# Performance work log

Hardware: AMD Instinct MI355X
Metric: run time of the kernel (lower is better)

## Reference

```python
import jax, jax.numpy as jnp
import numpy as np

LAMBDA_COLOR = 0.01
BLUR = 0.01          # geomloss blur
P = 2                # geomloss p
EPS_FINAL = BLUR ** P  # 1e-4
# Note: with scaling=1.2 (>1), geomloss's epsilon_schedule arange is empty, so
# eps_list = [diameter**p, blur**p] -> exactly two annealing stages.


def cost_matrix(x, y, lambda_color):
    # x: [B,N,6], y: [B,M,6]
    cx, col_x = x[..., :3], x[..., 3:]
    cy, col_y = y[..., :3], y[..., 3:]
    max_norm = jnp.max(jnp.linalg.norm(jnp.concatenate([cx, cy], axis=1), axis=-1))
    s = 1.0 / (max_norm + 1e-6)
    cxn, cyn = cx * s, cy * s
    coord = jnp.sum((cxn[:, :, None, :] - cyn[:, None, :, :]) ** 2, axis=-1)  # [B,N,M]
    col_x = jnp.clip(col_x, 0.0, 1.0)
    col_y = jnp.clip(col_y, 0.0, 1.0)
    col = jnp.sum((col_x[:, :, None, :] - col_y[:, None, :, :]) ** 2, axis=-1)
    return jnp.maximum(coord + lambda_color * col, 0.0)


def softmin(eps, C, h):
    # h: [B,M] = log_weights + potential/eps ; C: [B,N,M]
    return -eps * jax.nn.logsumexp(h[:, None, :] - C / eps, axis=2)  # [B,N]


def sinkhorn_distance(x, y, lambda_color):
    B, N, _ = x.shape
    M = y.shape[1]
    a_log = jnp.full((B, N), -np.log(N), dtype=x.dtype)
    b_log = jnp.full((B, M), -np.log(M), dtype=x.dtype)

    C_xy = cost_matrix(x, y, lambda_color)          # [B,N,M]
    C_yx = jnp.swapaxes(C_xy, 1, 2)                 # cost is symmetric in x<->y

    # diameter over raw 6-d features (geomloss max_diameter)
    pts = jnp.concatenate([x.reshape(-1, x.shape[-1]), y.reshape(-1, y.shape[-1])], axis=0)
    diameter = jnp.linalg.norm(pts.max(0) - pts.min(0))
    eps_list = (diameter ** P, jnp.asarray(EPS_FINAL, x.dtype))

    # Sinkhorn loop runs without gradient through the potentials (geomloss semantics)
    Cs_xy = jax.lax.stop_gradient(C_xy)
    Cs_yx = jax.lax.stop_gradient(C_yx)

    eps = eps_list[0]
    f = softmin(eps, Cs_xy, b_log)   # potential on x
    g = softmin(eps, Cs_yx, a_log)   # potential on y
    for eps in eps_list:
        ft = softmin(eps, Cs_xy, b_log + g / eps)
        gt = softmin(eps, Cs_yx, a_log + f / eps)
        f, g = 0.5 * (f + ft), 0.5 * (g + gt)

    # final extrapolation with gradient-carrying cost, detached dual potentials
    eps = eps_list[-1]
    f_new = softmin(eps, C_xy, b_log + jax.lax.stop_gradient(g) / eps)
    g_new = softmin(eps, C_yx, a_log + jax.lax.stop_gradient(f) / eps)

    # <a,f> + <b,g> with uniform weights
    ot = f_new.mean(axis=1) + g_new.mean(axis=1)   # [B]
    return ot.mean() * 10.0


def setup_inputs() -> dict:
    key = jax.random.key(0)
    kx, ky = jax.random.split(key)
    x = jax.random.normal(kx, (4, 4096, 6), dtype=jnp.float32)
    y = jax.random.normal(ky, (4, 4096, 6), dtype=jnp.float32)
    return {"x": x, "y": y}


def reference(x, y):
    return sinkhorn_distance(x, y, LAMBDA_COLOR)
```

## Files before the change

### kernel.cpp

```cpp
#include <hip/hip_runtime.h>

#define ROWS 16384
#define PTS_TOTAL 32768
#define NSM_BLK 512

#define LOG2E 1.4426950408889634f
#define LN2   0.6931471805599453f
#define NEG_LOG2M (-12.0f)
#define EPS1LNM 8.317766166719343e-4f

typedef _Float16 h2 __attribute__((ext_vector_type(2)));
typedef _Float16 v8h __attribute__((ext_vector_type(8)));
typedef float f32x4 __attribute__((ext_vector_type(4)));

__device__ inline float fexp2(float x) { return __builtin_amdgcn_exp2f(x); }
__device__ inline float flog2(float x) { return __builtin_amdgcn_logf(x); }

__device__ inline unsigned fenc(float f) {
  unsigned u = __float_as_uint(f);
  return (u & 0x80000000u) ? ~u : (u | 0x80000000u);
}
__device__ inline float fdec(unsigned u) {
  return (u & 0x80000000u) ? __uint_as_float(u & 0x7fffffffu)
                           : __uint_as_float(~u);
}
__device__ inline unsigned pkh2(float a, float b) {
  h2 hv; hv.x = (_Float16)a; hv.y = (_Float16)b;
  return __builtin_bit_cast(unsigned, hv);
}
__device__ inline v8h bcv8(uint4 u) { return __builtin_bit_cast(v8h, u); }

__device__ inline float mkv(const float* __restrict__ p, float s, float* v) {
  v[0] = p[0] * s; v[1] = p[1] * s; v[2] = p[2] * s;
  v[3] = 0.1f * fminf(fmaxf(p[3], 0.0f), 1.0f);
  v[4] = 0.1f * fminf(fmaxf(p[4], 0.0f), 1.0f);
  v[5] = 0.1f * fminf(fmaxf(p[5], 0.0f), 1.0f);
  return v[0]*v[0] + v[1]*v[1] + v[2]*v[2] + v[3]*v[3] + v[4]*v[4] + v[5]*v[5];
}

__device__ inline float taylor_f(const float* __restrict__ M, const float* v,
                                 float q, float eps0) {
  float sc2 = 2.0f * LOG2E / eps0;
  float p[6];
#pragma unroll
  for (int d = 0; d < 6; ++d) p[d] = v[d] * sc2;
  float t1 = 0.0f;
#pragma unroll
  for (int d = 0; d < 6; ++d) t1 += p[d] * M[1 + d];
  float t2 = 0.0f;
  int kk = 7;
#pragma unroll
  for (int d = 0; d < 6; ++d) {
#pragma unroll
    for (int e = d; e < 6; ++e) {
      float coef = (d == e) ? 1.0f : 2.0f;
      t2 += coef * p[d] * p[e] * M[kk];
      kk++;
    }
  }
  float S = M[0] + LN2 * t1 + (0.5f * LN2 * LN2) * t2;
  return q - eps0 * LN2 * flog2(S);
}

__device__ inline void mom28(float* acc, float wgt, const float* v) {
  acc[0] = wgt;
  int kk = 1;
#pragma unroll
  for (int d = 0; d < 6; ++d) acc[kk++] = wgt * v[d];
#pragma unroll
  for (int d = 0; d < 6; ++d) {
    float wv = wgt * v[d];
#pragma unroll
    for (int e = d; e < 6; ++e) acc[kk++] = wv * v[e];
  }
}

__device__ inline void red28g(float* acc, float* __restrict__ dst,
                              float (*shf)[28], int t, int wave, int lane) {
#pragma unroll
  for (int off = 32; off > 0; off >>= 1) {
#pragma unroll
    for (int k = 0; k < 28; ++k) acc[k] += __shfl_xor(acc[k], off);
  }
  if (lane == 0) {
#pragma unroll
    for (int k = 0; k < 28; ++k) shf[wave][k] = acc[k];
  }
  __syncthreads();
  if (t < 28) dst[t] = (shf[0][t] + shf[1][t]) + (shf[2][t] + shf[3][t]);
}

__device__ inline void se_from_rmax(const unsigned* __restrict__ RMAXu,
                                    unsigned (*shu)[13], float& s, float& eps0,
                                    int t, int wave, int lane) {
  int set = t & 127;
  unsigned e[13];
#pragma unroll
  for (int k = 0; k < 13; ++k) e[k] = RMAXu[set * 16 + k];
#pragma unroll
  for (int off = 32; off > 0; off >>= 1) {
#pragma unroll
    for (int k = 0; k < 13; ++k) {
      unsigned o = (unsigned)__shfl_xor((int)e[k], off);
      e[k] = e[k] > o ? e[k] : o;
    }
  }
  if (lane == 0) {
#pragma unroll
    for (int k = 0; k < 13; ++k) shu[wave][k] = e[k];
  }
  __syncthreads();
  unsigned mm[13];
#pragma unroll
  for (int k = 0; k < 13; ++k) {
    unsigned v0 = shu[0][k] > shu[1][k] ? shu[0][k] : shu[1][k];
    unsigned v1 = shu[2][k] > shu[3][k] ? shu[2][k] : shu[3][k];
    mm[k] = v0 > v1 ? v0 : v1;
  }
  s = 1.0f / (sqrtf(fdec(mm[0])) + 1e-6f);
  eps0 = 0.0f;
#pragma unroll
  for (int k = 0; k < 6; ++k) {
    float dd = fdec(mm[1 + k]) + fdec(mm[7 + k]);
    eps0 += dd * dd;
  }
}

__global__ __launch_bounds__(256) void k1_max(
    const float* __restrict__ x, const float* __restrict__ y,
    float* __restrict__ w) {
  unsigned* BARC = (unsigned*)w;
  unsigned* RMAX = (unsigned*)w + 64;
  const int t = threadIdx.x, wave = t >> 6, lane = t & 63, bx = blockIdx.x;
  if (bx == 0 && t == 0) BARC[0] = 0u;
  const int g0 = bx * 256;
  bool isx = g0 < ROWS;
  __shared__ float4 st[384];
  const float4* src =
      (const float4*)((isx ? x : y) + (size_t)(g0 & (ROWS - 1)) * 6);
  st[t] = src[t];
  if (t < 128) st[256 + t] = src[256 + t];
  __syncthreads();
  const float* sp = (const float*)st + t * 6;
  float d[6];
#pragma unroll
  for (int k = 0; k < 6; ++k) d[k] = sp[k];
  unsigned e[13];
  e[0] = fenc(d[0] * d[0] + d[1] * d[1] + d[2] * d[2]);
#pragma unroll
  for (int k = 0; k < 6; ++k) {
    e[1 + k] = fenc(d[k]);
    e[7 + k] = fenc(-d[k]);
  }
#pragma unroll
  for (int off = 32; off > 0; off >>= 1) {
#pragma unroll
    for (int k = 0; k < 13; ++k) {
      unsigned o = (unsigned)__shfl_xor((int)e[k], off);
      e[k] = e[k] > o ? e[k] : o;
    }
  }
  __shared__ unsigned shu[4][13];
  if (lane == 0) {
#pragma unroll
    for (int k = 0; k < 13; ++k) shu[wave][k] = e[k];
  }
  __syncthreads();
  if (t < 13) {
    unsigned v = shu[0][t];
#pragma unroll
    for (int wv = 1; wv < 4; ++wv) v = v > shu[wv][t] ? v : shu[wv][t];
    RMAX[bx * 16 + t] = v;
  }
}

__global__ __launch_bounds__(256) void k2_pack(
    const float* __restrict__ x, const float* __restrict__ y,
    float* __restrict__ w) {
  const int t = threadIdx.x, wave = t >> 6, lane = t & 63, bx = blockIdx.x;
  const unsigned* RMAX = (const unsigned*)w + 64;
  float* MOMP1 = w + 2560;
  float* base = w + 16384;
  uint4* AREC = (uint4*)base;
  float* Qarr = base + 3 * 4 * PTS_TOTAL;

  __shared__ unsigned shu[4][13];
  __shared__ float shf[4][28];
  float s, eps0;
  se_from_rmax(RMAX, shu, s, eps0, t, wave, lane);

  const int g = bx * 256 + t;
  const int side = g >> 14;
  const float* p = (side ? y : x) + (size_t)(g & (ROWS - 1)) * 6;
  float v[6]; float q = mkv(p, s, v);
  Qarr[g] = q;
  unsigned w01 = pkh2(v[0], v[1]), w23 = pkh2(v[2], v[3]), w45 = pkh2(v[4], v[5]);
  AREC[g] = (uint4){w01, w23, w45, pkh2(1.0f, 0.0f)};

  float wgt = fexp2(NEG_LOG2M - q * (LOG2E / eps0));
  float acc[28];
  mom28(acc, wgt, v);
  red28g(acc, MOMP1 + (size_t)bx * 32, shf, t, wave, lane);
}

__global__ __launch_bounds__(256) void k3_rows1(
    const float* __restrict__ x, const float* __restrict__ y,
    float* __restrict__ w) {
  const int t = threadIdx.x, wave = t >> 6, lane = t & 63, bx = blockIdx.x;
  const unsigned* RMAX = (const unsigned*)w + 64;
  const float* MOMP1 = w + 2560;
  float* MOMP2 = w + 2560 + 4096;
  float* base = w + 16384;
  float* FG1 = base + 3 * 4 * PTS_TOTAL + PTS_TOTAL + PTS_TOTAL;

  __shared__ unsigned shu[4][13];
  __shared__ float shf[4][28];
  __shared__ float M1opp[28];
  float s, eps0;
  se_from_rmax(RMAX, shu, s, eps0, t, wave, lane);

  const int g = bx * 256 + t;
  const int side = g >> 14;
  const int batch = (g >> 12) & 3;
  if (t < 28) {
    const float* mp = MOMP1 + ((size_t)((side ^ 1) * 64 + batch * 16)) * 32 + t;
    float m = 0.0f;
#pragma unroll
    for (int j = 0; j < 16; ++j) m += mp[j * 32];
    M1opp[t] = m;
  }
  __syncthreads();

  const float* p = (side ? y : x) + (size_t)(g & (ROWS - 1)) * 6;
  float v[6]; float q = mkv(p, s, v);
  float f1 = taylor_f(M1opp, v, q, eps0);
  FG1[g] = f1;
  float w2 = fexp2(NEG_LOG2M + (f1 - q) * (LOG2E / eps0));
  float acc[28];
  mom28(acc, w2, v);
  red28g(acc, MOMP2 + (size_t)bx * 32, shf, t, wave, lane);
}

__global__ __launch_bounds__(256) void k4_rows2(
    const float* __restrict__ x, const float* __restrict__ y,
    float* __restrict__ w) {
  const int t = threadIdx.x, wave = t >> 6, lane = t & 63, bx = blockIdx.x;
  const unsigned* RMAX = (const unsigned*)w + 64;
  const float* MOMP2 = w + 2560 + 4096;
  float* base = w + 16384;
  uint4* BRECA = (uint4*)base + PTS_TOTAL;
  float* Qarr = base + 3 * 4 * PTS_TOTAL;
  float* FG2 = Qarr + PTS_TOTAL;
  const float* FG1 = FG2 + PTS_TOTAL;

  __shared__ unsigned shu[4][13];
  __shared__ float M2opp[28];
  float s, eps0;
  se_from_rmax(RMAX, shu, s, eps0, t, wave, lane);

  const int g = bx * 256 + t;
  const int side = g >> 14;
  const int batch = (g >> 12) & 3;
  if (t < 28) {
    const float* mp = MOMP2 + ((size_t)((side ^ 1) * 64 + batch * 16)) * 32 + t;
    float m = 0.0f;
#pragma unroll
    for (int j = 0; j < 16; ++j) m += mp[j * 32];
    M2opp[t] = m;
  }
  __syncthreads();

  const float* p = (side ? y : x) + (size_t)(g & (ROWS - 1)) * 6;
  float v[6]; float q = mkv(p, s, v);
  float f1 = FG1[g];
  float f_t = taylor_f(M2opp, v, q, eps0);
  float f2 = 0.5f * (f1 + f_t);
  FG2[g] = f2;
  float hs2 = 0.5f * (f2 - q - EPS1LNM);
  unsigned w01 = pkh2(v[0], v[1]), w23 = pkh2(v[2], v[3]), w45 = pkh2(v[4], v[5]);
  BRECA[g] = (uint4){w01, w23, w45, pkh2(hs2, 0.0f)};
}

__device__ inline float softmax_max64L(const uint4* __restrict__ AREC,
                                       const uint4* __restrict__ BIN,
                                       uint4* __restrict__ Blds,
                                       float (*lm)[32]) {
  int t = threadIdx.x;
  int w = t >> 6, lane = t & 63;
  int l16 = lane & 15;
  bool ldq = lane < 16;
  int grow0 = blockIdx.x * 64;
  int side = grow0 >> 14;
  int batch = (grow0 & (ROWS - 1)) >> 12;
  int panel0 = (side ^ 1) * ROWS + batch * 4096;

  const uint4* gsrc = BIN + panel0 + w * 512 + lane;
  uint4* ldst = Blds + w * 512 + lane;
  uint4 s0 = gsrc[0],   s1 = gsrc[64],  s2 = gsrc[128], s3 = gsrc[192];
  uint4 s4 = gsrc[256], s5 = gsrc[320], s6 = gsrc[384], s7 = gsrc[448];

  uint4 z4 = (uint4){0u, 0u, 0u, 0u};
  uint4 a1u = z4, a2u = z4;
  int arow = grow0 + (w >> 2) * 32;
  if (ldq) {
    a1u = AREC[arow + l16];
    a2u = AREC[arow + 16 + l16];
  }
  v8h a1 = bcv8(a1u), a2 = bcv8(a2u);

  ldst[0] = s0;   ldst[64] = s1;  ldst[128] = s2; ldst[192] = s3;
  ldst[256] = s4; ldst[320] = s5; ldst[384] = s6; ldst[448] = s7;
  __syncthreads();

  f32x4 m2a = {-3.0e38f, -3.0e38f, -3.0e38f, -3.0e38f};
  f32x4 m2b = m2a;
  const f32x4 cz = {0.0f, 0.0f, 0.0f, 0.0f};
  const int colq = (w & 3) * 1024;

#pragma unroll 8
  for (int tt = 0; tt < 64; ++tt) {
    uint4 bu = z4;
    if (ldq) bu = Blds[colq + tt * 16 + l16];
    v8h b = bcv8(bu);
    f32x4 d1 = __builtin_amdgcn_mfma_f32_16x16x32_f16(a1, b, cz, 0, 0, 0);
    f32x4 d2 = __builtin_amdgcn_mfma_f32_16x16x32_f16(a2, b, cz, 0, 0, 0);
    m2a = __builtin_elementwise_max(m2a, d1);
    m2b = __builtin_elementwise_max(m2b, d2);
  }

#pragma unroll
  for (int off = 1; off <= 8; off <<= 1) {
#pragma unroll
    for (int r = 0; r < 4; ++r) {
      m2a[r] = fmaxf(m2a[r], __shfl_xor(m2a[r], off));
      m2b[r] = fmaxf(m2b[r], __shfl_xor(m2b[r], off));
    }
  }
  if (l16 == 0) {
    int qd = lane >> 4;
#pragma unroll
    for (int r = 0; r < 4; ++r) {
      lm[w][qd * 4 + r] = m2a[r];
      lm[w][16 + qd * 4 + r] = m2b[r];
    }
  }
  __syncthreads();
  float m = 0.0f;
  if (t < 64) {
    int half4 = (t >> 5) * 4, r32 = t & 31;
    m = fmaxf(fmaxf(lm[half4][r32], lm[half4 + 1][r32]),
              fmaxf(lm[half4 + 2][r32], lm[half4 + 3][r32]));
  }
  return m;
}

__global__ __launch_bounds__(512) void kb_sm1(
    const uint4* __restrict__ AREC, const uint4* __restrict__ BIN,
    uint4* __restrict__ BOUT, const float* __restrict__ Qarr,
    const float* __restrict__ FG2) {
  __shared__ uint4 Blds[4096];
  __shared__ float lm[8][32];
  int t = threadIdx.x;
  int grow0 = blockIdx.x * 64;
  float qv = 0.0f, fprev = 0.0f;
  uint4 ar = (uint4){0u, 0u, 0u, 0u};
  if (t < 64) {
    int gg = grow0 + t;
    qv = Qarr[gg];
    fprev = FG2[gg];
    ar = AREC[gg];
  }
  float m = softmax_max64L(AREC, BIN, Blds, lm);
  if (t < 64) {
    float f_t = qv - 2.0f * m;
    float fo = 0.5f * (fprev + f_t);
    float hs = 0.5f * (fo - qv - EPS1LNM);
    BOUT[grow0 + t] = (uint4){ar.x, ar.y, ar.z, pkh2(hs, 0.0f)};
  }
}

__global__ __launch_bounds__(512) void kc_sm2(
    const uint4* __restrict__ AREC, const uint4* __restrict__ BIN,
    const float* __restrict__ Qarr, float* __restrict__ PART,
    unsigned* __restrict__ BARC, float* __restrict__ out) {
  __shared__ uint4 Blds[4096];
  __shared__ float lm[8][32];
  __shared__ float fsh[64];
  __shared__ float fred[8];
  __shared__ int lastf;
  int t = threadIdx.x;
  int wave = t >> 6, lane = t & 63;
  int grow0 = blockIdx.x * 64;
  float qv = 0.0f;
  if (t < 64) qv = Qarr[grow0 + t];
  float m = softmax_max64L(AREC, BIN, Blds, lm);
  if (t < 64) fsh[t] = qv - 2.0f * m;
  __syncthreads();
  if (t == 0) {
    float ssum = 0.0f;
#pragma unroll
    for (int k = 0; k < 64; ++k) ssum += fsh[k];
    __hip_atomic_store(&PART[blockIdx.x], ssum, __ATOMIC_RELAXED,
                       __HIP_MEMORY_SCOPE_AGENT);
    unsigned old = __hip_atomic_fetch_add(BARC, 1u, __ATOMIC_ACQ_REL,
                                          __HIP_MEMORY_SCOPE_AGENT);
    lastf = (old == (unsigned)(NSM_BLK - 1)) ? 1 : 0;
  }
  __syncthreads();
  if (lastf) {
    float a = __hip_atomic_load(&PART[t], __ATOMIC_RELAXED,
                                __HIP_MEMORY_SCOPE_AGENT);
#pragma unroll
    for (int off = 32; off > 0; off >>= 1) a += __shfl_xor(a, off);
    if (lane == 0) fred[wave] = a;
    __syncthreads();
    if (t == 0) {
      float s8 = 0.0f;
#pragma unroll
      for (int k = 0; k < 8; ++k) s8 += fred[k];
      out[0] = s8 * (10.0f / (float)ROWS);
    }
  }
}

extern "C" void kernel_launch(void* const* d_in, const int* in_sizes, int n_in,
                              void* d_out, int out_size, void* d_ws,
                              size_t ws_size, hipStream_t stream) {
  const float* x = (const float*)d_in[0];
  const float* y = (const float*)d_in[1];
  float* out = (float*)d_out;
  float* w = (float*)d_ws;

  unsigned* BARC = (unsigned*)w;
  float* base = w + 16384;
  uint4* AREC  = (uint4*)base;
  uint4* BRECA = AREC + PTS_TOTAL;
  uint4* BRECB = BRECA + PTS_TOTAL;
  float* Qarr  = base + 3 * 4 * PTS_TOTAL;
  float* FG2   = Qarr + PTS_TOTAL;
  float* FG1   = FG2 + PTS_TOTAL;
  float* PART  = FG1 + PTS_TOTAL;

  (void)ws_size;
  k1_max<<<128, 256, 0, stream>>>(x, y, w);
  k2_pack<<<128, 256, 0, stream>>>(x, y, w);
  k3_rows1<<<128, 256, 0, stream>>>(x, y, w);
  k4_rows2<<<128, 256, 0, stream>>>(x, y, w);
  kb_sm1<<<NSM_BLK, 512, 0, stream>>>(AREC, BRECA, BRECB, Qarr, FG2);
  kc_sm2<<<NSM_BLK, 512, 0, stream>>>(AREC, BRECB, Qarr, PART, BARC, out);
}
```

Baseline: 99.65 us.

## Fuse four preprocessing kernels into one with grid-wide atomic barriers

```diff
diff --git a/kernel.cpp b/kernel.cpp
--- a/kernel.cpp
+++ b/kernel.cpp
@@ -3,6 +3,7 @@
 #define ROWS 16384
 #define PTS_TOTAL 32768
 #define NSM_BLK 512
+#define NEPS_BLK 128
 
 #define LOG2E 1.4426950408889634f
 #define LN2   0.6931471805599453f
@@ -30,11 +31,11 @@
 }
 __device__ inline v8h bcv8(uint4 u) { return __builtin_bit_cast(v8h, u); }
 
-__device__ inline float mkv(const float* __restrict__ p, float s, float* v) {
-  v[0] = p[0] * s; v[1] = p[1] * s; v[2] = p[2] * s;
-  v[3] = 0.1f * fminf(fmaxf(p[3], 0.0f), 1.0f);
-  v[4] = 0.1f * fminf(fmaxf(p[4], 0.0f), 1.0f);
-  v[5] = 0.1f * fminf(fmaxf(p[5], 0.0f), 1.0f);
+__device__ inline float mkv_d(const float* d, float s, float* v) {
+  v[0] = d[0] * s; v[1] = d[1] * s; v[2] = d[2] * s;
+  v[3] = 0.1f * fminf(fmaxf(d[3], 0.0f), 1.0f);
+  v[4] = 0.1f * fminf(fmaxf(d[4], 0.0f), 1.0f);
+  v[5] = 0.1f * fminf(fmaxf(d[5], 0.0f), 1.0f);
   return v[0]*v[0] + v[1]*v[1] + v[2]*v[2] + v[3]*v[3] + v[4]*v[4] + v[5]*v[5];
 }
 
@@ -75,67 +76,50 @@
   }
 }
 
-__device__ inline void red28g(float* acc, float* __restrict__ dst,
-                              float (*shf)[28], int t, int wave, int lane) {
-#pragma unroll
-  for (int off = 32; off > 0; off >>= 1) {
-#pragma unroll
-    for (int k = 0; k < 28; ++k) acc[k] += __shfl_xor(acc[k], off);
-  }
-  if (lane == 0) {
-#pragma unroll
-    for (int k = 0; k < 28; ++k) shf[wave][k] = acc[k];
-  }
-  __syncthreads();
-  if (t < 28) dst[t] = (shf[0][t] + shf[1][t]) + (shf[2][t] + shf[3][t]);
-}
-
-__device__ inline void se_from_rmax(const unsigned* __restrict__ RMAXu,
-                                    unsigned (*shu)[13], float& s, float& eps0,
-                                    int t, int wave, int lane) {
-  int set = t & 127;
-  unsigned e[13];
-#pragma unroll
-  for (int k = 0; k < 13; ++k) e[k] = RMAXu[set * 16 + k];
-#pragma unroll
-  for (int off = 32; off > 0; off >>= 1) {
-#pragma unroll
-    for (int k = 0; k < 13; ++k) {
-      unsigned o = (unsigned)__shfl_xor((int)e[k], off);
-      e[k] = e[k] > o ? e[k] : o;
-    }
-  }
-  if (lane == 0) {
-#pragma unroll
-    for (int k = 0; k < 13; ++k) shu[wave][k] = e[k];
-  }
-  __syncthreads();
-  unsigned mm[13];
-#pragma unroll
-  for (int k = 0; k < 13; ++k) {
-    unsigned v0 = shu[0][k] > shu[1][k] ? shu[0][k] : shu[1][k];
-    unsigned v1 = shu[2][k] > shu[3][k] ? shu[2][k] : shu[3][k];
-    mm[k] = v0 > v1 ? v0 : v1;
-  }
-  s = 1.0f / (sqrtf(fdec(mm[0])) + 1e-6f);
-  eps0 = 0.0f;
-#pragma unroll
-  for (int k = 0; k < 6; ++k) {
-    float dd = fdec(mm[1 + k]) + fdec(mm[7 + k]);
-    eps0 += dd * dd;
-  }
-}
-
-__global__ __launch_bounds__(256) void k1_max(
+__device__ inline void lite_bar(unsigned* c, unsigned n) {
+  __syncthreads();
+  if (threadIdx.x == 0) {
+    __hip_atomic_fetch_add(c, 1u, __ATOMIC_ACQ_REL, __HIP_MEMORY_SCOPE_AGENT);
+    while (__hip_atomic_load(c, __ATOMIC_ACQUIRE, __HIP_MEMORY_SCOPE_AGENT) < n)
+      __builtin_amdgcn_s_sleep(4);
+  }
+  __syncthreads();
+}
+
+__global__ __launch_bounds__(256) void k0_init(float* __restrict__ w) {
+  int t = threadIdx.x;
+  unsigned* u = (unsigned*)w;
+  if (t < 4) u[t] = 0u;
+  if (t < 128) u[64 + t] = 0u;
+  w[2560 + t] = 0.0f;
+  w[2816 + t] = 0.0f;
+}
+
+__global__ __launch_bounds__(256) void k_eps0(
     const float* __restrict__ x, const float* __restrict__ y,
     float* __restrict__ w) {
-  unsigned* BARC = (unsigned*)w;
-  unsigned* RMAX = (unsigned*)w + 64;
   const int t = threadIdx.x, wave = t >> 6, lane = t & 63, bx = blockIdx.x;
-  if (bx == 0 && t == 0) BARC[0] = 0u;
+  unsigned* CNT = (unsigned*)w;
+  unsigned* ENC = (unsigned*)w + 64;
+  float* MOM1 = w + 2560;
+  float* MOM2 = w + 2816;
+  float* base = w + 16384;
+  uint4* AREC  = (uint4*)base;
+  uint4* BRECA = (uint4*)base + PTS_TOTAL;
+  float* Qarr  = base + 3 * 4 * PTS_TOTAL;
+  float* FG2   = Qarr + PTS_TOTAL;
+
+  const int g = bx * 256 + t;
   const int g0 = bx * 256;
+  const int side = g0 >> 14;
+  const int batch = (g0 >> 12) & 3;
+
+  __shared__ float4 st[384];
+  __shared__ unsigned shu[4][13];
+  __shared__ float shf[4][28];
+  __shared__ float Msh[28];
+
   bool isx = g0 < ROWS;
-  __shared__ float4 st[384];
   const float4* src =
       (const float4*)((isx ? x : y) + (size_t)(g0 & (ROWS - 1)) * 6);
   st[t] = src[t];
@@ -145,139 +129,112 @@
   float d[6];
 #pragma unroll
   for (int k = 0; k < 6; ++k) d[k] = sp[k];
-  unsigned e[13];
-  e[0] = fenc(d[0] * d[0] + d[1] * d[1] + d[2] * d[2]);
-#pragma unroll
-  for (int k = 0; k < 6; ++k) {
-    e[1 + k] = fenc(d[k]);
-    e[7 + k] = fenc(-d[k]);
-  }
-#pragma unroll
-  for (int off = 32; off > 0; off >>= 1) {
-#pragma unroll
-    for (int k = 0; k < 13; ++k) {
-      unsigned o = (unsigned)__shfl_xor((int)e[k], off);
-      e[k] = e[k] > o ? e[k] : o;
-    }
-  }
-  __shared__ unsigned shu[4][13];
-  if (lane == 0) {
-#pragma unroll
-    for (int k = 0; k < 13; ++k) shu[wave][k] = e[k];
-  }
-  __syncthreads();
-  if (t < 13) {
-    unsigned v = shu[0][t];
-#pragma unroll
-    for (int wv = 1; wv < 4; ++wv) v = v > shu[wv][t] ? v : shu[wv][t];
-    RMAX[bx * 16 + t] = v;
-  }
-}
-
-__global__ __launch_bounds__(256) void k2_pack(
-    const float* __restrict__ x, const float* __restrict__ y,
-    float* __restrict__ w) {
-  const int t = threadIdx.x, wave = t >> 6, lane = t & 63, bx = blockIdx.x;
-  const unsigned* RMAX = (const unsigned*)w + 64;
-  float* MOMP1 = w + 2560;
-  float* base = w + 16384;
-  uint4* AREC = (uint4*)base;
-  float* Qarr = base + 3 * 4 * PTS_TOTAL;
-
-  __shared__ unsigned shu[4][13];
-  __shared__ float shf[4][28];
+  {
+    unsigned e[13];
+    e[0] = fenc(d[0] * d[0] + d[1] * d[1] + d[2] * d[2]);
+#pragma unroll
+    for (int k = 0; k < 6; ++k) {
+      e[1 + k] = fenc(d[k]);
+      e[7 + k] = fenc(-d[k]);
+    }
+#pragma unroll
+    for (int off = 32; off > 0; off >>= 1) {
+#pragma unroll
+      for (int k = 0; k < 13; ++k) {
+        unsigned o = (unsigned)__shfl_xor((int)e[k], off);
+        e[k] = e[k] > o ? e[k] : o;
+      }
+    }
+    if (lane == 0) {
+#pragma unroll
+      for (int k = 0; k < 13; ++k) shu[wave][k] = e[k];
+    }
+    __syncthreads();
+    if (t < 13) {
+      unsigned v = shu[0][t];
+#pragma unroll
+      for (int wv = 1; wv < 4; ++wv) v = v > shu[wv][t] ? v : shu[wv][t];
+      atomicMax(&ENC[t * 8], v);
+    }
+  }
+  lite_bar(CNT + 0, NEPS_BLK);
+  if (t < 13)
+    shu[0][t] = __hip_atomic_load(&ENC[t * 8], __ATOMIC_RELAXED,
+                                  __HIP_MEMORY_SCOPE_AGENT);
+  __syncthreads();
   float s, eps0;
-  se_from_rmax(RMAX, shu, s, eps0, t, wave, lane);
-
-  const int g = bx * 256 + t;
-  const int side = g >> 14;
-  const float* p = (side ? y : x) + (size_t)(g & (ROWS - 1)) * 6;
-  float v[6]; float q = mkv(p, s, v);
+  {
+    s = 1.0f / (sqrtf(fdec(shu[0][0])) + 1e-6f);
+    eps0 = 0.0f;
+#pragma unroll
+    for (int k = 0; k < 6; ++k) {
+      float dd = fdec(shu[0][1 + k]) + fdec(shu[0][7 + k]);
+      eps0 += dd * dd;
+    }
+  }
+
+  float v[6];
+  float q = mkv_d(d, s, v);
+  {
+    float wgt = fexp2(NEG_LOG2M - q * (LOG2E / eps0));
+    float acc[28];
+    mom28(acc, wgt, v);
+#pragma unroll
+    for (int off = 32; off > 0; off >>= 1) {
+#pragma unroll
+      for (int k = 0; k < 28; ++k) acc[k] += __shfl_xor(acc[k], off);
+    }
+    if (lane == 0) {
+#pragma unroll
+      for (int k = 0; k < 28; ++k) shf[wave][k] = acc[k];
+    }
+    __syncthreads();
+    if (t < 28) {
+      float vv = (shf[0][t] + shf[1][t]) + (shf[2][t] + shf[3][t]);
+      __hip_atomic_fetch_add(&MOM1[(side * 4 + batch) * 32 + t], vv,
+                             __ATOMIC_RELAXED, __HIP_MEMORY_SCOPE_AGENT);
+    }
+  }
+  lite_bar(CNT + 1, NEPS_BLK);
+  if (t < 28)
+    Msh[t] = __hip_atomic_load(&MOM1[((side ^ 1) * 4 + batch) * 32 + t],
+                               __ATOMIC_RELAXED, __HIP_MEMORY_SCOPE_AGENT);
+  __syncthreads();
+  float f1 = taylor_f(Msh, v, q, eps0);
+
+  {
+    float w2 = fexp2(NEG_LOG2M + (f1 - q) * (LOG2E / eps0));
+    float acc[28];
+    mom28(acc, w2, v);
+#pragma unroll
+    for (int off = 32; off > 0; off >>= 1) {
+#pragma unroll
+      for (int k = 0; k < 28; ++k) acc[k] += __shfl_xor(acc[k], off);
+    }
+    if (lane == 0) {
+#pragma unroll
+      for (int k = 0; k < 28; ++k) shf[wave][k] = acc[k];
+    }
+    __syncthreads();
+    if (t < 28) {
+      float vv = (shf[0][t] + shf[1][t]) + (shf[2][t] + shf[3][t]);
+      __hip_atomic_fetch_add(&MOM2[(side * 4 + batch) * 32 + t], vv,
+                             __ATOMIC_RELAXED, __HIP_MEMORY_SCOPE_AGENT);
+    }
+  }
+  lite_bar(CNT + 2, NEPS_BLK);
+  if (t < 28)
+    Msh[t] = __hip_atomic_load(&MOM2[((side ^ 1) * 4 + batch) * 32 + t],
+                               __ATOMIC_RELAXED, __HIP_MEMORY_SCOPE_AGENT);
+  __syncthreads();
+
+  float f_t = taylor_f(Msh, v, q, eps0);
+  float f2 = 0.5f * (f1 + f_t);
   Qarr[g] = q;
+  FG2[g] = f2;
   unsigned w01 = pkh2(v[0], v[1]), w23 = pkh2(v[2], v[3]), w45 = pkh2(v[4], v[5]);
   AREC[g] = (uint4){w01, w23, w45, pkh2(1.0f, 0.0f)};
-
-  float wgt = fexp2(NEG_LOG2M - q * (LOG2E / eps0));
-  float acc[28];
-  mom28(acc, wgt, v);
-  red28g(acc, MOMP1 + (size_t)bx * 32, shf, t, wave, lane);
-}
-
-__global__ __launch_bounds__(256) void k3_rows1(
-    const float* __restrict__ x, const float* __restrict__ y,
-    float* __restrict__ w) {
-  const int t = threadIdx.x, wave = t >> 6, lane = t & 63, bx = blockIdx.x;
-  const unsigned* RMAX = (const unsigned*)w + 64;
-  const float* MOMP1 = w + 2560;
-  float* MOMP2 = w + 2560 + 4096;
-  float* base = w + 16384;
-  float* FG1 = base + 3 * 4 * PTS_TOTAL + PTS_TOTAL + PTS_TOTAL;
-
-  __shared__ unsigned shu[4][13];
-  __shared__ float shf[4][28];
-  __shared__ float M1opp[28];
-  float s, eps0;
-  se_from_rmax(RMAX, shu, s, eps0, t, wave, lane);
-
-  const int g = bx * 256 + t;
-  const int side = g >> 14;
-  const int batch = (g >> 12) & 3;
-  if (t < 28) {
-    const float* mp = MOMP1 + ((size_t)((side ^ 1) * 64 + batch * 16)) * 32 + t;
-    float m = 0.0f;
-#pragma unroll
-    for (int j = 0; j < 16; ++j) m += mp[j * 32];
-    M1opp[t] = m;
-  }
-  __syncthreads();
-
-  const float* p = (side ? y : x) + (size_t)(g & (ROWS - 1)) * 6;
-  float v[6]; float q = mkv(p, s, v);
-  float f1 = taylor_f(M1opp, v, q, eps0);
-  FG1[g] = f1;
-  float w2 = fexp2(NEG_LOG2M + (f1 - q) * (LOG2E / eps0));
-  float acc[28];
-  mom28(acc, w2, v);
-  red28g(acc, MOMP2 + (size_t)bx * 32, shf, t, wave, lane);
-}
-
-__global__ __launch_bounds__(256) void k4_rows2(
-    const float* __restrict__ x, const float* __restrict__ y,
-    float* __restrict__ w) {
-  const int t = threadIdx.x, wave = t >> 6, lane = t & 63, bx = blockIdx.x;
-  const unsigned* RMAX = (const unsigned*)w + 64;
-  const float* MOMP2 = w + 2560 + 4096;
-  float* base = w + 16384;
-  uint4* BRECA = (uint4*)base + PTS_TOTAL;
-  float* Qarr = base + 3 * 4 * PTS_TOTAL;
-  float* FG2 = Qarr + PTS_TOTAL;
-  const float* FG1 = FG2 + PTS_TOTAL;
-
-  __shared__ unsigned shu[4][13];
-  __shared__ float M2opp[28];
-  float s, eps0;
-  se_from_rmax(RMAX, shu, s, eps0, t, wave, lane);
-
-  const int g = bx * 256 + t;
-  const int side = g >> 14;
-  const int batch = (g >> 12) & 3;
-  if (t < 28) {
-    const float* mp = MOMP2 + ((size_t)((side ^ 1) * 64 + batch * 16)) * 32 + t;
-    float m = 0.0f;
-#pragma unroll
-    for (int j = 0; j < 16; ++j) m += mp[j * 32];
-    M2opp[t] = m;
-  }
-  __syncthreads();
-
-  const float* p = (side ? y : x) + (size_t)(g & (ROWS - 1)) * 6;
-  float v[6]; float q = mkv(p, s, v);
-  float f1 = FG1[g];
-  float f_t = taylor_f(M2opp, v, q, eps0);
-  float f2 = 0.5f * (f1 + f_t);
-  FG2[g] = f2;
   float hs2 = 0.5f * (f2 - q - EPS1LNM);
-  unsigned w01 = pkh2(v[0], v[1]), w23 = pkh2(v[2], v[3]), w45 = pkh2(v[4], v[5]);
   BRECA[g] = (uint4){w01, w23, w45, pkh2(hs2, 0.0f)};
 }
 
@@ -431,21 +388,18 @@
   float* out = (float*)d_out;
   float* w = (float*)d_ws;
 
-  unsigned* BARC = (unsigned*)w;
+  unsigned* BARC = (unsigned*)w + 3;
   float* base = w + 16384;
   uint4* AREC  = (uint4*)base;
   uint4* BRECA = AREC + PTS_TOTAL;
   uint4* BRECB = BRECA + PTS_TOTAL;
   float* Qarr  = base + 3 * 4 * PTS_TOTAL;
   float* FG2   = Qarr + PTS_TOTAL;
-  float* FG1   = FG2 + PTS_TOTAL;
-  float* PART  = FG1 + PTS_TOTAL;
+  float* PART  = FG2 + PTS_TOTAL;
 
   (void)ws_size;
-  k1_max<<<128, 256, 0, stream>>>(x, y, w);
-  k2_pack<<<128, 256, 0, stream>>>(x, y, w);
-  k3_rows1<<<128, 256, 0, stream>>>(x, y, w);
-  k4_rows2<<<128, 256, 0, stream>>>(x, y, w);
+  k0_init<<<1, 256, 0, stream>>>(w);
+  k_eps0<<<NEPS_BLK, 256, 0, stream>>>(x, y, w);
   kb_sm1<<<NSM_BLK, 512, 0, stream>>>(AREC, BRECA, BRECB, Qarr, FG2);
   kc_sm2<<<NSM_BLK, 512, 0, stream>>>(AREC, BRECB, Qarr, PART, BARC, out);
 }
```

Result: slower. 112.4 us (+12.8%).

## Fuse second Taylor stage into first softmax kernel and drop k4 launch

Applied to the files above, without the earlier changes.

```diff
diff --git a/kernel.cpp b/kernel.cpp
--- a/kernel.cpp
+++ b/kernel.cpp
@@ -38,8 +38,8 @@
   return v[0]*v[0] + v[1]*v[1] + v[2]*v[2] + v[3]*v[3] + v[4]*v[4] + v[5]*v[5];
 }
 
-__device__ inline float taylor_f(const float* __restrict__ M, const float* v,
-                                 float q, float eps0) {
+__device__ inline float taylor_fmq(const float* __restrict__ M, const float* v,
+                                   float eps0) {
   float sc2 = 2.0f * LOG2E / eps0;
   float p[6];
 #pragma unroll
@@ -59,7 +59,11 @@
     }
   }
   float S = M[0] + LN2 * t1 + (0.5f * LN2 * LN2) * t2;
-  return q - eps0 * LN2 * flog2(S);
+  return -eps0 * LN2 * flog2(S);
+}
+__device__ inline float taylor_f(const float* __restrict__ M, const float* v,
+                                 float q, float eps0) {
+  return q + taylor_fmq(M, v, eps0);
 }
 
 __device__ inline void mom28(float* acc, float wgt, const float* v) {
@@ -188,6 +192,7 @@
   __shared__ float shf[4][28];
   float s, eps0;
   se_from_rmax(RMAX, shu, s, eps0, t, wave, lane);
+  if (bx == 0 && t == 0) { w[32] = s; w[33] = eps0; }
 
   const int g = bx * 256 + t;
   const int side = g >> 14;
@@ -210,8 +215,6 @@
   const unsigned* RMAX = (const unsigned*)w + 64;
   const float* MOMP1 = w + 2560;
   float* MOMP2 = w + 2560 + 4096;
-  float* base = w + 16384;
-  float* FG1 = base + 3 * 4 * PTS_TOTAL + PTS_TOTAL + PTS_TOTAL;
 
   __shared__ unsigned shu[4][13];
   __shared__ float shf[4][28];
@@ -234,88 +237,91 @@
   const float* p = (side ? y : x) + (size_t)(g & (ROWS - 1)) * 6;
   float v[6]; float q = mkv(p, s, v);
   float f1 = taylor_f(M1opp, v, q, eps0);
-  FG1[g] = f1;
   float w2 = fexp2(NEG_LOG2M + (f1 - q) * (LOG2E / eps0));
   float acc[28];
   mom28(acc, w2, v);
   red28g(acc, MOMP2 + (size_t)bx * 32, shf, t, wave, lane);
 }
 
-__global__ __launch_bounds__(256) void k4_rows2(
+__global__ __launch_bounds__(512) void kb_sm1(
     const float* __restrict__ x, const float* __restrict__ y,
-    float* __restrict__ w) {
-  const int t = threadIdx.x, wave = t >> 6, lane = t & 63, bx = blockIdx.x;
-  const unsigned* RMAX = (const unsigned*)w + 64;
-  const float* MOMP2 = w + 2560 + 4096;
-  float* base = w + 16384;
-  uint4* BRECA = (uint4*)base + PTS_TOTAL;
-  float* Qarr = base + 3 * 4 * PTS_TOTAL;
-  float* FG2 = Qarr + PTS_TOTAL;
-  const float* FG1 = FG2 + PTS_TOTAL;
-
-  __shared__ unsigned shu[4][13];
-  __shared__ float M2opp[28];
-  float s, eps0;
-  se_from_rmax(RMAX, shu, s, eps0, t, wave, lane);
-
-  const int g = bx * 256 + t;
-  const int side = g >> 14;
-  const int batch = (g >> 12) & 3;
-  if (t < 28) {
-    const float* mp = MOMP2 + ((size_t)((side ^ 1) * 64 + batch * 16)) * 32 + t;
-    float m = 0.0f;
-#pragma unroll
-    for (int j = 0; j < 16; ++j) m += mp[j * 32];
-    M2opp[t] = m;
-  }
-  __syncthreads();
-
-  const float* p = (side ? y : x) + (size_t)(g & (ROWS - 1)) * 6;
-  float v[6]; float q = mkv(p, s, v);
-  float f1 = FG1[g];
-  float f_t = taylor_f(M2opp, v, q, eps0);
-  float f2 = 0.5f * (f1 + f_t);
-  FG2[g] = f2;
-  float hs2 = 0.5f * (f2 - q - EPS1LNM);
-  unsigned w01 = pkh2(v[0], v[1]), w23 = pkh2(v[2], v[3]), w45 = pkh2(v[4], v[5]);
-  BRECA[g] = (uint4){w01, w23, w45, pkh2(hs2, 0.0f)};
-}
-
-__device__ inline float softmax_max64L(const uint4* __restrict__ AREC,
-                                       const uint4* __restrict__ BIN,
-                                       uint4* __restrict__ Blds,
-                                       float (*lm)[32]) {
-  int t = threadIdx.x;
-  int w = t >> 6, lane = t & 63;
-  int l16 = lane & 15;
-  bool ldq = lane < 16;
-  int grow0 = blockIdx.x * 64;
-  int side = grow0 >> 14;
-  int batch = (grow0 & (ROWS - 1)) >> 12;
-  int panel0 = (side ^ 1) * ROWS + batch * 4096;
-
-  const uint4* gsrc = BIN + panel0 + w * 512 + lane;
-  uint4* ldst = Blds + w * 512 + lane;
+    const uint4* __restrict__ AREC, float* __restrict__ H3,
+    const float* __restrict__ w) {
+  __shared__ uint4 Blds[4096];
+  __shared__ float lm[8][32];
+  __shared__ float M1own[28], M1opp[28], M2own[28], M2opp[28];
+  const int t = threadIdx.x;
+  const int wv = t >> 6, lane = t & 63;
+  const int l16 = lane & 15;
+  const bool ldq = lane < 16;
+  const int grow0 = blockIdx.x * 64;
+  const int side = grow0 >> 14;
+  const int batch = (grow0 & (ROWS - 1)) >> 12;
+  const int panel0 = (side ^ 1) * ROWS + batch * 4096;
+
+  const float s = w[32], eps0 = w[33];
+
+  const uint4* gsrc = AREC + panel0 + wv * 512 + lane;
   uint4 s0 = gsrc[0],   s1 = gsrc[64],  s2 = gsrc[128], s3 = gsrc[192];
   uint4 s4 = gsrc[256], s5 = gsrc[320], s6 = gsrc[384], s7 = gsrc[448];
 
+  const float* MOMP1 = w + 2560;
+  const float* MOMP2 = w + 2560 + 4096;
+  if (wv < 4 && lane < 28) {
+    int msde = (wv & 1) ? (side ^ 1) : side;
+    const float* MP = (wv < 2) ? MOMP1 : MOMP2;
+    const float* mp = MP + ((size_t)(msde * 64 + batch * 16)) * 32 + lane;
+    float m = 0.0f;
+#pragma unroll
+    for (int j = 0; j < 16; ++j) m += mp[j * 32];
+    float* dst = (wv == 0) ? M1own : (wv == 1) ? M1opp
+               : (wv == 2) ? M2own : M2opp;
+    dst[lane] = m;
+  }
+  __syncthreads();
+
+  float f2imq = 0.0f;
+  if (t < 64) {
+    int gg = grow0 + t;
+    const float* p = (side ? y : x) + (size_t)(gg & (ROWS - 1)) * 6;
+    float v[6]; (void)mkv(p, s, v);
+    float fmq1 = taylor_fmq(M1opp, v, eps0);
+    float fmq2 = taylor_fmq(M2opp, v, eps0);
+    f2imq = 0.5f * (fmq1 + fmq2);
+  }
+
+  auto patch = [&](uint4 su) -> uint4 {
+    h2 ha = __builtin_bit_cast(h2, su.x);
+    h2 hb = __builtin_bit_cast(h2, su.y);
+    h2 hc = __builtin_bit_cast(h2, su.z);
+    float v[6] = {(float)ha.x, (float)ha.y, (float)hb.x,
+                  (float)hb.y, (float)hc.x, (float)hc.y};
+    float fmq1 = taylor_fmq(M1own, v, eps0);
+    float fmq2 = taylor_fmq(M2own, v, eps0);
+    float hs2 = 0.25f * (fmq1 + fmq2) - 0.5f * EPS1LNM;
+    su.w = pkh2(hs2, 0.0f);
+    return su;
+  };
+  uint4* ldst = Blds + wv * 512 + lane;
+  ldst[0] = patch(s0);   ldst[64] = patch(s1);
+  ldst[128] = patch(s2); ldst[192] = patch(s3);
+  ldst[256] = patch(s4); ldst[320] = patch(s5);
+  ldst[384] = patch(s6); ldst[448] = patch(s7);
+
   uint4 z4 = (uint4){0u, 0u, 0u, 0u};
   uint4 a1u = z4, a2u = z4;
-  int arow = grow0 + (w >> 2) * 32;
+  int arow = grow0 + (wv >> 2) * 32;
   if (ldq) {
     a1u = AREC[arow + l16];
     a2u = AREC[arow + 16 + l16];
   }
   v8h a1 = bcv8(a1u), a2 = bcv8(a2u);
-
-  ldst[0] = s0;   ldst[64] = s1;  ldst[128] = s2; ldst[192] = s3;
-  ldst[256] = s4; ldst[320] = s5; ldst[384] = s6; ldst[448] = s7;
   __syncthreads();
 
   f32x4 m2a = {-3.0e38f, -3.0e38f, -3.0e38f, -3.0e38f};
   f32x4 m2b = m2a;
   const f32x4 cz = {0.0f, 0.0f, 0.0f, 0.0f};
-  const int colq = (w & 3) * 1024;
+  const int colq = (wv & 3) * 1024;
 
 #pragma unroll 8
   for (int tt = 0; tt < 64; ++tt) {
@@ -327,7 +333,6 @@
     m2a = __builtin_elementwise_max(m2a, d1);
     m2b = __builtin_elementwise_max(m2b, d2);
   }
-
 #pragma unroll
   for (int off = 1; off <= 8; off <<= 1) {
 #pragma unroll
@@ -340,47 +345,21 @@
     int qd = lane >> 4;
 #pragma unroll
     for (int r = 0; r < 4; ++r) {
-      lm[w][qd * 4 + r] = m2a[r];
-      lm[w][16 + qd * 4 + r] = m2b[r];
-    }
-  }
-  __syncthreads();
-  float m = 0.0f;
+      lm[wv][qd * 4 + r] = m2a[r];
+      lm[wv][16 + qd * 4 + r] = m2b[r];
+    }
+  }
+  __syncthreads();
   if (t < 64) {
     int half4 = (t >> 5) * 4, r32 = t & 31;
-    m = fmaxf(fmaxf(lm[half4][r32], lm[half4 + 1][r32]),
-              fmaxf(lm[half4 + 2][r32], lm[half4 + 3][r32]));
-  }
-  return m;
-}
-
-__global__ __launch_bounds__(512) void kb_sm1(
-    const uint4* __restrict__ AREC, const uint4* __restrict__ BIN,
-    uint4* __restrict__ BOUT, const float* __restrict__ Qarr,
-    const float* __restrict__ FG2) {
-  __shared__ uint4 Blds[4096];
-  __shared__ float lm[8][32];
-  int t = threadIdx.x;
-  int grow0 = blockIdx.x * 64;
-  float qv = 0.0f, fprev = 0.0f;
-  uint4 ar = (uint4){0u, 0u, 0u, 0u};
-  if (t < 64) {
-    int gg = grow0 + t;
-    qv = Qarr[gg];
-    fprev = FG2[gg];
-    ar = AREC[gg];
-  }
-  float m = softmax_max64L(AREC, BIN, Blds, lm);
-  if (t < 64) {
-    float f_t = qv - 2.0f * m;
-    float fo = 0.5f * (fprev + f_t);
-    float hs = 0.5f * (fo - qv - EPS1LNM);
-    BOUT[grow0 + t] = (uint4){ar.x, ar.y, ar.z, pkh2(hs, 0.0f)};
+    float m = fmaxf(fmaxf(lm[half4][r32], lm[half4 + 1][r32]),
+                    fmaxf(lm[half4 + 2][r32], lm[half4 + 3][r32]));
+    H3[grow0 + t] = 0.5f * (0.5f * f2imq - m - EPS1LNM);
   }
 }
 
 __global__ __launch_bounds__(512) void kc_sm2(
-    const uint4* __restrict__ AREC, const uint4* __restrict__ BIN,
+    const uint4* __restrict__ AREC, const float* __restrict__ H3,
     const float* __restrict__ Qarr, float* __restrict__ PART,
     unsigned* __restrict__ BARC, float* __restrict__ out) {
   __shared__ uint4 Blds[4096];
@@ -388,13 +367,81 @@
   __shared__ float fsh[64];
   __shared__ float fred[8];
   __shared__ int lastf;
-  int t = threadIdx.x;
-  int wave = t >> 6, lane = t & 63;
-  int grow0 = blockIdx.x * 64;
+  const int t = threadIdx.x;
+  const int wv = t >> 6, lane = t & 63;
+  const int l16 = lane & 15;
+  const bool ldq = lane < 16;
+  const int grow0 = blockIdx.x * 64;
+  const int side = grow0 >> 14;
+  const int batch = (grow0 & (ROWS - 1)) >> 12;
+  const int panel0 = (side ^ 1) * ROWS + batch * 4096;
+
+  const uint4* gsrc = AREC + panel0 + wv * 512 + lane;
+  const float* h3p = H3 + panel0 + wv * 512 + lane;
+  uint4 s0 = gsrc[0],   s1 = gsrc[64],  s2 = gsrc[128], s3 = gsrc[192];
+  uint4 s4 = gsrc[256], s5 = gsrc[320], s6 = gsrc[384], s7 = gsrc[448];
+  float h0 = h3p[0],   h1 = h3p[64],  h2v = h3p[128], h3v = h3p[192];
+  float h4 = h3p[256], h5 = h3p[320], h6 = h3p[384],  h7 = h3p[448];
+
   float qv = 0.0f;
   if (t < 64) qv = Qarr[grow0 + t];
-  float m = softmax_max64L(AREC, BIN, Blds, lm);
-  if (t < 64) fsh[t] = qv - 2.0f * m;
+
+  s0.w = pkh2(h0, 0.0f);  s1.w = pkh2(h1, 0.0f);
+  s2.w = pkh2(h2v, 0.0f); s3.w = pkh2(h3v, 0.0f);
+  s4.w = pkh2(h4, 0.0f);  s5.w = pkh2(h5, 0.0f);
+  s6.w = pkh2(h6, 0.0f);  s7.w = pkh2(h7, 0.0f);
+  uint4* ldst = Blds + wv * 512 + lane;
+  ldst[0] = s0;   ldst[64] = s1;  ldst[128] = s2; ldst[192] = s3;
+  ldst[256] = s4; ldst[320] = s5; ldst[384] = s6; ldst[448] = s7;
+
+  uint4 z4 = (uint4){0u, 0u, 0u, 0u};
+  uint4 a1u = z4, a2u = z4;
+  int arow = grow0 + (wv >> 2) * 32;
+  if (ldq) {
+    a1u = AREC[arow + l16];
+    a2u = AREC[arow + 16 + l16];
+  }
+  v8h a1 = bcv8(a1u), a2 = bcv8(a2u);
+  __syncthreads();
+
+  f32x4 m2a = {-3.0e38f, -3.0e38f, -3.0e38f, -3.0e38f};
+  f32x4 m2b = m2a;
+  const f32x4 cz = {0.0f, 0.0f, 0.0f, 0.0f};
+  const int colq = (wv & 3) * 1024;
+
+#pragma unroll 8
+  for (int tt = 0; tt < 64; ++tt) {
+    uint4 bu = z4;
+    if (ldq) bu = Blds[colq + tt * 16 + l16];
+    v8h b = bcv8(bu);
+    f32x4 d1 = __builtin_amdgcn_mfma_f32_16x16x32_f16(a1, b, cz, 0, 0, 0);
+    f32x4 d2 = __builtin_amdgcn_mfma_f32_16x16x32_f16(a2, b, cz, 0, 0, 0);
+    m2a = __builtin_elementwise_max(m2a, d1);
+    m2b = __builtin_elementwise_max(m2b, d2);
+  }
+#pragma unroll
+  for (int off = 1; off <= 8; off <<= 1) {
+#pragma unroll
+    for (int r = 0; r < 4; ++r) {
+      m2a[r] = fmaxf(m2a[r], __shfl_xor(m2a[r], off));
+      m2b[r] = fmaxf(m2b[r], __shfl_xor(m2b[r], off));
+    }
+  }
+  if (l16 == 0) {
+    int qd = lane >> 4;
+#pragma unroll
+    for (int r = 0; r < 4; ++r) {
+      lm[wv][qd * 4 + r] = m2a[r];
+      lm[wv][16 + qd * 4 + r] = m2b[r];
+    }
+  }
+  __syncthreads();
+  if (t < 64) {
+    int half4 = (t >> 5) * 4, r32 = t & 31;
+    float m = fmaxf(fmaxf(lm[half4][r32], lm[half4 + 1][r32]),
+                    fmaxf(lm[half4 + 2][r32], lm[half4 + 3][r32]));
+    fsh[t] = qv - 2.0f * m;
+  }
   __syncthreads();
   if (t == 0) {
     float ssum = 0.0f;
@@ -412,7 +459,7 @@
                                 __HIP_MEMORY_SCOPE_AGENT);
 #pragma unroll
     for (int off = 32; off > 0; off >>= 1) a += __shfl_xor(a, off);
-    if (lane == 0) fred[wave] = a;
+    if (lane == 0) fred[wv] = a;
     __syncthreads();
     if (t == 0) {
       float s8 = 0.0f;
@@ -433,19 +480,15 @@
 
   unsigned* BARC = (unsigned*)w;
   float* base = w + 16384;
-  uint4* AREC  = (uint4*)base;
-  uint4* BRECA = AREC + PTS_TOTAL;
-  uint4* BRECB = BRECA + PTS_TOTAL;
-  float* Qarr  = base + 3 * 4 * PTS_TOTAL;
-  float* FG2   = Qarr + PTS_TOTAL;
-  float* FG1   = FG2 + PTS_TOTAL;
-  float* PART  = FG1 + PTS_TOTAL;
+  uint4* AREC = (uint4*)base;
+  float* H3   = base + 4 * PTS_TOTAL;
+  float* Qarr = base + 3 * 4 * PTS_TOTAL;
+  float* PART = Qarr + 3 * PTS_TOTAL;
 
   (void)ws_size;
   k1_max<<<128, 256, 0, stream>>>(x, y, w);
   k2_pack<<<128, 256, 0, stream>>>(x, y, w);
   k3_rows1<<<128, 256, 0, stream>>>(x, y, w);
-  k4_rows2<<<128, 256, 0, stream>>>(x, y, w);
-  kb_sm1<<<NSM_BLK, 512, 0, stream>>>(AREC, BRECA, BRECB, Qarr, FG2);
-  kc_sm2<<<NSM_BLK, 512, 0, stream>>>(AREC, BRECB, Qarr, PART, BARC, out);
-}
+  kb_sm1<<<NSM_BLK, 512, 0, stream>>>(x, y, AREC, H3, w);
+  kc_sm2<<<NSM_BLK, 512, 0, stream>>>(AREC, H3, Qarr, PART, BARC, out);
+}
```

Result: slower. 103.5 us (+3.9%).
